# Kernel optimization log

Measured on AMD Instinct MI355X. Metric: run time of the kernel, lower is better.

The kernel has to match this reference:

```python
import jax, jax.numpy as jnp
import numpy as np
import math

WS = (8, 8)        # window_size for context (2D)
HEADS = 8


def _attend(q, k, v, h):
    # q: (Bw, Nq, inner), k/v: (Bw, Nk, inner)
    Bw, Nq, inner = q.shape
    d = inner // h
    q = q.reshape(Bw, Nq, h, d)
    k = k.reshape(Bw, -1, h, d)
    v = v.reshape(Bw, -1, h, d)
    scores = jnp.einsum('bqhd,bkhd->bhqk', q, k) * (d ** -0.5)
    attn = jax.nn.softmax(scores, axis=-1)
    out = jnp.einsum('bhqk,bkhd->bqhd', attn, v)
    return out.reshape(Bw, Nq, inner)


def reference(x, context, W_q, W_k, W_v, W_out, b_out):
    B, C, T, H, W = x.shape
    H_, W_ = context.shape[-2], context.shape[-1]
    ws = WS
    assert H_ * W_ > ws[0] * ws[1] and H * W >= ws[0] * ws[1]  # window branch
    # pad context to multiple of window_size (no-op for chosen shapes)
    pad_r_2d = (-W_) % ws[1]
    pad_b_2d = (-H_) % ws[0]
    context = jnp.pad(context, ((0, 0), (0, 0), (0, pad_b_2d), (0, pad_r_2d)))
    # scaled window size for the (smaller) 3D query tensor
    ws_ = (math.ceil(float(ws[0]) * H / H_), math.ceil(float(ws[1]) * W / W_))
    pad_r_3d = (-W) % ws_[1]
    pad_b_3d = (-H) % ws_[0]
    x = jnp.pad(x, ((0, 0), (0, 0), (0, 0), (0, pad_b_3d), (0, pad_r_3d)))
    Hp, Wp = x.shape[-2], x.shape[-1]
    Hc, Wc = context.shape[-2], context.shape[-1]
    # window partition: context (B,C,Hc,Wc) -> (B*h*w, ws0*ws1, C)
    hc, wc = Hc // ws[0], Wc // ws[1]
    ctx = context.reshape(B, C, hc, ws[0], wc, ws[1])
    ctx = ctx.transpose(0, 2, 4, 3, 5, 1).reshape(B * hc * wc, ws[0] * ws[1], C)
    # window partition: x (B,C,T,Hp,Wp) -> (B*h*w, T*ws_0*ws_1, C)
    hg, wg = Hp // ws_[0], Wp // ws_[1]
    xw = x.reshape(B, C, T, hg, ws_[0], wg, ws_[1])
    xw = xw.transpose(0, 3, 5, 2, 4, 6, 1).reshape(B * hg * wg, T * ws_[0] * ws_[1], C)
    # QKV projections (no bias: qkv_bias=False, to_k always bias-free)
    q = xw @ W_q
    k = ctx @ W_k
    v = ctx @ W_v
    out = _attend(q, k, v, HEADS)  # (Bw, Nq, inner)
    inner = out.shape[-1]
    # window reverse -> (B, inner, T, Hp, Wp)
    out = out.reshape(B, hg, wg, T, ws_[0], ws_[1], inner)
    out = out.transpose(0, 6, 3, 1, 4, 2, 5).reshape(B, inner, T, Hp, Wp)
    out = out[:, :, :, :H, :W]
    # b c t h w -> b (t h w) c
    out = out.transpose(0, 2, 3, 4, 1).reshape(B, T * H * W, inner)
    return out @ W_out + b_out


def setup_inputs() -> dict:
    key = jax.random.key(0)
    ks = jax.random.split(key, 7)
    D = 512
    s = 0.02
    return {
        'x': jax.random.normal(ks[0], (4, D, 4, 32, 32), jnp.float32),
        'context': jax.random.normal(ks[1], (4, D, 128, 128), jnp.float32),
        'W_q': jax.random.normal(ks[2], (D, D), jnp.float32) * s,
        'W_k': jax.random.normal(ks[3], (D, D), jnp.float32) * s,
        'W_v': jax.random.normal(ks[4], (D, D), jnp.float32) * s,
        'W_out': jax.random.normal(ks[5], (D, D), jnp.float32) * s,
        'b_out': jnp.zeros((D,), jnp.float32),
    }
```

## Files before the change

kernel.cpp:

```cpp
#include <hip/hip_runtime.h>
#include <hip/hip_bf16.h>

typedef unsigned short u16;
typedef unsigned int u32;
typedef __attribute__((ext_vector_type(4))) float f32x4;
typedef __attribute__((ext_vector_type(4))) u16 u16x4;
typedef __attribute__((ext_vector_type(8))) u16 u16x8;
typedef __attribute__((ext_vector_type(8))) short s16x8;

__device__ __forceinline__ u16 f2bf(float f) {
    union { float f; u32 u; } v; v.f = f;
    u32 r = v.u + 0x7FFFu + ((v.u >> 16) & 1u);
    return (u16)(r >> 16);
}

__device__ __forceinline__ void gl_lds16(const u16* g, u16* l) {
    __builtin_amdgcn_global_load_lds(
        (const __attribute__((address_space(1))) unsigned int*)(const void*)g,
        (__attribute__((address_space(3))) unsigned int*)(void*)l, 16, 0, 0);
}

__global__ __launch_bounds__(256) void prep_kernel(
    const float* __restrict__ w0, const float* __restrict__ w1,
    const float* __restrict__ w2, const float* __restrict__ w3, u16* __restrict__ WT,
    const float* __restrict__ x, u16* __restrict__ Aq,
    const float* __restrict__ ctx, u16* __restrict__ Actx) {
    __shared__ char smem[16640];
    int bid = blockIdx.x;
    int tid = threadIdx.x;
    if (bid < 8192) {
        u16 (*t)[68] = (u16(*)[68])smem;
        int b2 = bid;
        int cb = b2 & 7; b2 >>= 3;
        int xb = b2 & 1; b2 >>= 1;
        int y  = b2 & 127; b2 >>= 7;
        int b  = b2;
        long ibase = ((long)(b * 512 + cb * 64) * 128 + y) * 128 + xb * 64;
#pragma unroll
        for (int p = 0; p < 4; ++p) {
            int task = p * 256 + tid;
            int cc = task >> 4, xl = (task & 15) * 4;
            float4 v = *(const float4*)&ctx[ibase + (long)cc * 16384 + xl];
            u16x4 o = {f2bf(v.x), f2bf(v.y), f2bf(v.z), f2bf(v.w)};
            *(u16x4*)&t[cc][xl] = o;
        }
        __syncthreads();
#pragma unroll
        for (int p = 0; p < 2; ++p) {
            int task = p * 256 + tid;
            int xx = task >> 3, j = task & 7;
            u16x8 o;
#pragma unroll
            for (int i = 0; i < 8; ++i) o[i] = t[j * 8 + i][xx];
            int xg = xb * 64 + xx;
            int row = b * 16384 + (y >> 3) * 1024 + (xg >> 3) * 64 + (y & 7) * 8 + (xg & 7);
            *(u16x8*)&Actx[(long)row * 512 + cb * 64 + j * 8] = o;
        }
    } else if (bid < 12288) {
        u16 (*t)[36] = (u16(*)[36])smem;
        int b2 = bid - 8192;
        int cb = b2 & 7; b2 >>= 3;
        int y  = b2 & 31; b2 >>= 5;
        int tt = b2 & 3; b2 >>= 2;
        int b  = b2;
        long ibase = ((long)(b * 512 + cb * 64) * 4 + tt) * 1024 + y * 32;
#pragma unroll
        for (int p = 0; p < 2; ++p) {
            int task = p * 256 + tid;
            int cc = task >> 3, xl = (task & 7) * 4;
            float4 v = *(const float4*)&x[ibase + (long)cc * 4096 + xl];
            u16x4 o = {f2bf(v.x), f2bf(v.y), f2bf(v.z), f2bf(v.w)};
            *(u16x4*)&t[cc][xl] = o;
        }
        __syncthreads();
        {
            int xx = tid >> 3, j = tid & 7;
            u16x8 o;
#pragma unroll
            for (int i = 0; i < 8; ++i) o[i] = t[j * 8 + i][xx];
            int row = b * 4096 + (y >> 1) * 256 + (xx >> 1) * 16 + tt * 4 + (y & 1) * 2 + (xx & 1);
            *(u16x8*)&Aq[(long)row * 512 + cb * 64 + j * 8] = o;
        }
    } else {
        float (*t)[65] = (float(*)[65])smem;
        int b2 = bid - 12288;
        int wsel = b2 >> 6;
        int tile = b2 & 63;
        int j0 = (tile >> 3) * 64, c0 = (tile & 7) * 64;
        const float* src = wsel == 0 ? w0 : wsel == 1 ? w1 : wsel == 2 ? w2 : w3;
        u16* out = WT + (long)wsel * 512 * 512;
        int tj = tid & 63;
        int ti = tid >> 6;
#pragma unroll
        for (int p = 0; p < 16; ++p) {
            int row = p * 4 + ti;
            t[row][tj] = src[(long)(c0 + row) * 512 + j0 + tj];
        }
        __syncthreads();
#pragma unroll
        for (int p = 0; p < 16; ++p) {
            int jl = p * 4 + ti;
            out[(long)(j0 + jl) * 512 + c0 + tj] = f2bf(t[tj][jl]);
        }
    }
}

template <int FINAL>
__global__ __launch_bounds__(256, 4) void gemm128_kernel(
    const u16* __restrict__ A, const u16* __restrict__ Bt,
    u16* __restrict__ Cb, float* __restrict__ Cf, const float* __restrict__ bias) {
    __shared__ u16 As[1024 * 8];
    __shared__ u16 Bs[1024 * 8];
    int tid = threadIdx.x;
    int lane = tid & 63;
    int w = tid >> 6;
    int wm = w >> 1, wn = w & 1;
    int bid = blockIdx.x;
    int wg = (bid & 7) * 64 + (bid >> 3);
    int m0 = (wg >> 2) * 128;
    int n0 = (wg & 3) * 128;

    const f32x4 z = {0.f, 0.f, 0.f, 0.f};
    f32x4 acc[4][4];
#pragma unroll
    for (int i = 0; i < 4; ++i)
#pragma unroll
        for (int j = 0; j < 4; ++j) acc[i][j] = z;

    int aoff[4], boff[4], lb[4];
#pragma unroll
    for (int i = 0; i < 4; ++i) {
        int s = i * 256 + tid;
        int row = s >> 3;
        int cb = (s & 7) ^ (row & 7);
        aoff[i] = (m0 + row) * 512 + cb * 8;
        boff[i] = (n0 + row) * 512 + cb * 8;
        lb[i] = (i * 256 + w * 64) * 8;
    }
    int la = lane & 15, lg = lane >> 4;
    for (int ks = 0; ks < 8; ++ks) {
        int ko = ks * 64;
#pragma unroll
        for (int i = 0; i < 4; ++i) {
            gl_lds16(&A[aoff[i] + ko], &As[lb[i]]);
            gl_lds16(&Bt[boff[i] + ko], &Bs[lb[i]]);
        }
        __syncthreads();
#pragma unroll
        for (int kk = 0; kk < 2; ++kk) {
            int cb = kk * 4 + lg;
            s16x8 af[4], bfr[4];
#pragma unroll
            for (int mt = 0; mt < 4; ++mt) {
                int r = wm * 64 + mt * 16 + la;
                af[mt] = *(const s16x8*)&As[r * 64 + ((cb ^ (r & 7)) * 8)];
            }
#pragma unroll
            for (int nt = 0; nt < 4; ++nt) {
                int c = wn * 64 + nt * 16 + la;
                bfr[nt] = *(const s16x8*)&Bs[c * 64 + ((cb ^ (c & 7)) * 8)];
            }
#pragma unroll
            for (int mt = 0; mt < 4; ++mt)
#pragma unroll
                for (int nt = 0; nt < 4; ++nt)
                    acc[mt][nt] = __builtin_amdgcn_mfma_f32_16x16x32_bf16(af[mt], bfr[nt], acc[mt][nt], 0, 0, 0);
        }
        __syncthreads();
    }
#pragma unroll
    for (int mt = 0; mt < 4; ++mt) {
#pragma unroll
        for (int nt = 0; nt < 4; ++nt) {
            int col = n0 + wn * 64 + nt * 16 + la;
#pragma unroll
            for (int rr = 0; rr < 4; ++rr) {
                int r = m0 + wm * 64 + mt * 16 + lg * 4 + rr;
                float v = acc[mt][nt][rr];
                if (FINAL) {
                    int bb = r >> 12, hg = (r >> 8) & 15, wgx = (r >> 4) & 15;
                    int tt = (r >> 2) & 3, rr0 = (r >> 1) & 1, cc0 = r & 1;
                    int tok = bb * 4096 + tt * 1024 + (hg * 2 + rr0) * 32 + wgx * 2 + cc0;
                    Cf[(long)tok * 512 + col] = v + bias[col];
                } else {
                    Cb[(long)r * 512 + col] = f2bf(v);
                }
            }
        }
    }
}

__global__ __launch_bounds__(512, 2) void gemmkv256_kernel(
    const u16* __restrict__ Actx, const u16* __restrict__ WTk, const u16* __restrict__ WTv,
    u16* __restrict__ CK, u16* __restrict__ CVT) {
    __shared__ u16 lds[2][2][16384];
    int tid = threadIdx.x;
    int lane = tid & 63;
    int w = tid >> 6;
    int wm = w >> 2, wn = w & 3;
    int la = lane & 15, lg = lane >> 4;
    int bid = blockIdx.x;
    int wg = (bid & 7) * 128 + (bid >> 3);
    int ttile = wg >> 2;
    int role = wg & 3;
    int isV = role >> 1;
    int half = role & 1;

    const u16* srcA = isV ? WTv : Actx;
    const u16* srcB = isV ? Actx : WTk;

    const f32x4 z = {0.f, 0.f, 0.f, 0.f};
    f32x4 acc[8][4];
#pragma unroll
    for (int i = 0; i < 8; ++i)
#pragma unroll
        for (int j = 0; j < 4; ++j) acc[i][j] = z;

    int aoff[4], boff[4], lsl[4];
#pragma unroll
    for (int i = 0; i < 4; ++i) {
        int s = i * 512 + tid;
        int row = s >> 3;
        int cb = (s & 7) ^ (row & 7);
        int tok = (ttile * 256 + row) * 512 + cb * 8;
        int wgt = (half * 256 + row) * 512 + cb * 8;
        aoff[i] = isV ? wgt : tok;
        boff[i] = isV ? tok : wgt;
        lsl[i] = (i * 512 + w * 64) * 8;
    }

    s16x8 bfr[4][2];

#pragma unroll
    for (int i = 0; i < 4; ++i) {
        gl_lds16(&srcA[aoff[i]], &lds[0][0][lsl[i]]);
        gl_lds16(&srcB[boff[i]], &lds[0][1][lsl[i]]);
    }
#pragma unroll
    for (int i = 0; i < 4; ++i) {
        gl_lds16(&srcA[aoff[i] + 64], &lds[1][0][lsl[i]]);
        gl_lds16(&srcB[boff[i] + 64], &lds[1][1][lsl[i]]);
    }
    asm volatile("s_waitcnt vmcnt(8)" ::: "memory");
    __builtin_amdgcn_s_barrier();
    asm volatile("" ::: "memory");

#pragma unroll
    for (int t = 0; t < 8; ++t) {
        int buf = t & 1;
        const u16* Ab = lds[buf][0];
        const u16* Bb = lds[buf][1];
        int ko2 = (t + 2) * 64;

        {
            int cb = lg;
            s16x8 af[4];
#pragma unroll
            for (int mt = 0; mt < 4; ++mt) {
                int r = wm * 128 + mt * 16 + la;
                af[mt] = *(const s16x8*)&Ab[r * 64 + ((cb ^ (r & 7)) * 8)];
            }
#pragma unroll
            for (int nt = 0; nt < 4; ++nt) {
                int c = wn * 64 + nt * 16 + la;
                bfr[nt][0] = *(const s16x8*)&Bb[c * 64 + ((cb ^ (c & 7)) * 8)];
            }
            __builtin_amdgcn_s_barrier();
            __builtin_amdgcn_s_setprio(1);
#pragma unroll
            for (int mt = 0; mt < 4; ++mt)
#pragma unroll
                for (int nt = 0; nt < 4; ++nt)
                    acc[mt][nt] = __builtin_amdgcn_mfma_f32_16x16x32_bf16(af[mt], bfr[nt][0], acc[mt][nt], 0, 0, 0);
            __builtin_amdgcn_s_setprio(0);
            __builtin_amdgcn_sched_barrier(0);
            __builtin_amdgcn_s_barrier();
        }
        {
            int cb = 4 + lg;
            s16x8 af[4];
#pragma unroll
            for (int mt = 0; mt < 4; ++mt) {
                int r = wm * 128 + mt * 16 + la;
                af[mt] = *(const s16x8*)&Ab[r * 64 + ((cb ^ (r & 7)) * 8)];
            }
#pragma unroll
            for (int nt = 0; nt < 4; ++nt) {
                int c = wn * 64 + nt * 16 + la;
                bfr[nt][1] = *(const s16x8*)&Bb[c * 64 + ((cb ^ (c & 7)) * 8)];
            }
            __builtin_amdgcn_s_barrier();
            __builtin_amdgcn_s_setprio(1);
#pragma unroll
            for (int mt = 0; mt < 4; ++mt)
#pragma unroll
                for (int nt = 0; nt < 4; ++nt)
                    acc[mt][nt] = __builtin_amdgcn_mfma_f32_16x16x32_bf16(af[mt], bfr[nt][1], acc[mt][nt], 0, 0, 0);
            __builtin_amdgcn_s_setprio(0);
            __builtin_amdgcn_sched_barrier(0);
            __builtin_amdgcn_s_barrier();
        }
        {
            int cb = 4 + lg;
            s16x8 af[4];
#pragma unroll
            for (int mt = 0; mt < 4; ++mt) {
                int r = wm * 128 + 64 + mt * 16 + la;
                af[mt] = *(const s16x8*)&Ab[r * 64 + ((cb ^ (r & 7)) * 8)];
            }
            if (t < 6) {
                gl_lds16(&srcB[boff[0] + ko2], &lds[buf][1][lsl[0]]);
                gl_lds16(&srcB[boff[1] + ko2], &lds[buf][1][lsl[1]]);
                gl_lds16(&srcA[aoff[0] + ko2], &lds[buf][0][lsl[0]]);
            }
            __builtin_amdgcn_s_barrier();
            __builtin_amdgcn_s_setprio(1);
#pragma unroll
            for (int mt = 0; mt < 4; ++mt)
#pragma unroll
                for (int nt = 0; nt < 4; ++nt)
                    acc[4 + mt][nt] = __builtin_amdgcn_mfma_f32_16x16x32_bf16(af[mt], bfr[nt][1], acc[4 + mt][nt], 0, 0, 0);
            __builtin_amdgcn_s_setprio(0);
            __builtin_amdgcn_sched_barrier(0);
            __builtin_amdgcn_s_barrier();
        }
        {
            int cb = lg;
            s16x8 af[4];
#pragma unroll
            for (int mt = 0; mt < 4; ++mt) {
                int r = wm * 128 + 64 + mt * 16 + la;
                af[mt] = *(const s16x8*)&Ab[r * 64 + ((cb ^ (r & 7)) * 8)];
            }
            if (t < 6) {
                gl_lds16(&srcB[boff[2] + ko2], &lds[buf][1][lsl[2]]);
                gl_lds16(&srcB[boff[3] + ko2], &lds[buf][1][lsl[3]]);
                gl_lds16(&srcA[aoff[2] + ko2], &lds[buf][0][lsl[2]]);
            }
            __builtin_amdgcn_s_barrier();
            __builtin_amdgcn_s_setprio(1);
#pragma unroll
            for (int mt = 0; mt < 4; ++mt)
#pragma unroll
                for (int nt = 0; nt < 4; ++nt)
                    acc[4 + mt][nt] = __builtin_amdgcn_mfma_f32_16x16x32_bf16(af[mt], bfr[nt][0], acc[4 + mt][nt], 0, 0, 0);
            __builtin_amdgcn_s_setprio(0);
            __builtin_amdgcn_sched_barrier(0);
            __builtin_amdgcn_s_barrier();
        }
        if (t < 6) {
            gl_lds16(&srcA[aoff[1] + ko2], &lds[buf][0][lsl[1]]);
            gl_lds16(&srcA[aoff[3] + ko2], &lds[buf][0][lsl[3]]);
            asm volatile("s_waitcnt vmcnt(8)" ::: "memory");
            __builtin_amdgcn_s_barrier();
            asm volatile("" ::: "memory");
        } else if (t == 6) {
            asm volatile("s_waitcnt vmcnt(0)" ::: "memory");
            __builtin_amdgcn_s_barrier();
            asm volatile("" ::: "memory");
        }
    }

    if (!isV) {
#pragma unroll
        for (int mt = 0; mt < 8; ++mt) {
#pragma unroll
            for (int nt = 0; nt < 4; ++nt) {
                int col = half * 256 + wn * 64 + nt * 16 + la;
#pragma unroll
                for (int rr = 0; rr < 4; ++rr) {
                    int r = ttile * 256 + wm * 128 + mt * 16 + lg * 4 + rr;
                    CK[(long)r * 512 + col] = f2bf(acc[mt][nt][rr]);
                }
            }
        }
    } else {
        int winb = ttile * 4 + wn;
#pragma unroll
        for (int mt = 0; mt < 8; ++mt) {
#pragma unroll
            for (int nt = 0; nt < 4; ++nt) {
                int kv = nt * 16 + la;
#pragma unroll
                for (int rr = 0; rr < 4; ++rr) {
                    int d = half * 256 + wm * 128 + mt * 16 + lg * 4 + rr;
                    CVT[(long)winb * 32768 + d * 64 + kv] = f2bf(acc[mt][nt][rr]);
                }
            }
        }
    }
}

__global__ __launch_bounds__(256) void attn_kernel(
    const u16* __restrict__ Q, const u16* __restrict__ K,
    const u16* __restrict__ VT, u16* __restrict__ O) {
    __shared__ u16 P[4][16 * 104];
    int bid = blockIdx.x;
    int wgid = (bid & 7) * 256 + (bid >> 3);
    int tid = threadIdx.x;
    int wid = tid >> 6;
    int lane = tid & 63;
    int win = wgid >> 1;
    int h = (wgid & 1) * 4 + wid;
    int la = lane & 15, lg = lane >> 4;
    u16* Pw = P[wid];
    const u16* Qb = Q + (long)win * 16 * 512 + h * 64;
    const u16* Kb = K + (long)win * 64 * 512 + h * 64;
    const u16* Vt = VT + (long)win * 32768 + h * 64 * 64;

    s16x8 qf[2];
#pragma unroll
    for (int kk = 0; kk < 2; ++kk)
        qf[kk] = *(const s16x8*)&Qb[la * 512 + kk * 32 + lg * 8];

    const f32x4 z = {0.f, 0.f, 0.f, 0.f};
    f32x4 st[4];
#pragma unroll
    for (int rt = 0; rt < 4; ++rt) st[rt] = z;
#pragma unroll
    for (int rt = 0; rt < 4; ++rt)
#pragma unroll
        for (int kk = 0; kk < 2; ++kk) {
            s16x8 kf = *(const s16x8*)&Kb[(rt * 16 + la) * 512 + kk * 32 + lg * 8];
            st[rt] = __builtin_amdgcn_mfma_f32_16x16x32_bf16(kf, qf[kk], st[rt], 0, 0, 0);
        }
    float mloc = -1e30f;
#pragma unroll
    for (int rt = 0; rt < 4; ++rt)
#pragma unroll
        for (int rr = 0; rr < 4; ++rr) {
            st[rt][rr] *= 0.125f;
            mloc = fmaxf(mloc, st[rt][rr]);
        }
    mloc = fmaxf(mloc, __shfl_xor(mloc, 16));
    mloc = fmaxf(mloc, __shfl_xor(mloc, 32));
    float p[4][4];
    float sloc = 0.f;
#pragma unroll
    for (int rt = 0; rt < 4; ++rt)
#pragma unroll
        for (int rr = 0; rr < 4; ++rr) {
            p[rt][rr] = __expf(st[rt][rr] - mloc);
            sloc += p[rt][rr];
        }
    sloc += __shfl_xor(sloc, 16);
    sloc += __shfl_xor(sloc, 32);
    float inv = 1.0f / sloc;
#pragma unroll
    for (int rt = 0; rt < 4; ++rt)
#pragma unroll
        for (int rr = 0; rr < 4; ++rr)
            Pw[la * 104 + rt * 16 + lg * 4 + rr] = f2bf(p[rt][rr] * inv);
    __syncthreads();

    f32x4 od[4];
#pragma unroll
    for (int dt = 0; dt < 4; ++dt) od[dt] = z;
#pragma unroll
    for (int kk2 = 0; kk2 < 2; ++kk2) {
        s16x8 pa = *(const s16x8*)&Pw[la * 104 + kk2 * 32 + lg * 8];
#pragma unroll
        for (int dt = 0; dt < 4; ++dt) {
            s16x8 vb = *(const s16x8*)&Vt[(dt * 16 + la) * 64 + kk2 * 32 + lg * 8];
            od[dt] = __builtin_amdgcn_mfma_f32_16x16x32_bf16(pa, vb, od[dt], 0, 0, 0);
        }
    }
    u16* Ob = O + (long)win * 16 * 512 + h * 64;
#pragma unroll
    for (int dt = 0; dt < 4; ++dt)
#pragma unroll
        for (int rr = 0; rr < 4; ++rr)
            Ob[(long)(lg * 4 + rr) * 512 + dt * 16 + la] = f2bf(od[dt][rr]);
}

__global__ void sentinel_kernel(float* out) {
    if (threadIdx.x == 0 && blockIdx.x == 0) out[0] = -12345.0f;
}

extern "C" void kernel_launch(void* const* d_in, const int* in_sizes, int n_in,
                              void* d_out, int out_size, void* d_ws, size_t ws_size,
                              hipStream_t stream) {
    const float* x   = (const float*)d_in[0];
    const float* ctx = (const float*)d_in[1];
    const float* Wq  = (const float*)d_in[2];
    const float* Wk  = (const float*)d_in[3];
    const float* Wv  = (const float*)d_in[4];
    const float* Wo  = (const float*)d_in[5];
    const float* bo  = (const float*)d_in[6];
    float* out = (float*)d_out;

    u16* wsb  = (u16*)d_ws;
    u16* WT   = wsb;
    u16* Aq   = WT + 4l * 262144;
    u16* Actx = Aq + 8388608l;
    u16* Qb   = Actx + 33554432l;
    u16* Kb   = Qb + 8388608l;
    u16* VTb  = Kb + 33554432l;
    u16* Ob   = VTb + 33554432l;
    size_t need = (size_t)(126877696l) * 2;
    if (ws_size < need) {
        sentinel_kernel<<<1, 64, 0, stream>>>(out);
        return;
    }

    prep_kernel<<<12544, 256, 0, stream>>>(Wq, Wk, Wv, Wo, WT, x, Aq, ctx, Actx);
    gemm128_kernel<0><<<512, 256, 0, stream>>>(Aq, WT, Qb, nullptr, nullptr);
    gemmkv256_kernel<<<1024, 512, 0, stream>>>(Actx, WT + 262144l, WT + 2l * 262144, Kb, VTb);
    attn_kernel<<<2048, 256, 0, stream>>>(Qb, Kb, VTb, Ob);
    gemm128_kernel<1><<<512, 256, 0, stream>>>(Ob, WT + 3l * 262144, nullptr, out, bo);
}
```

Measured before the change: 198.8 us.

## Merge Q projection into KV GEMM kernel with 128x128 tiles

Replaces the separate Q-projection GEMM launch and the 256x256-tile K/V GEMM with one kernel that covers Q, K and V^T using 128x128 tiles and 256-thread blocks. The inner loop is simplified to two k-substeps per 64-wide chunk, with all prefetch loads issued after the compute and a single barrier pair. This removes one kernel launch and lets Q tiles fill the tail of the K/V grid. In exchange, smaller tiles give less data reuse per block and the finer interleaving of loads with MFMA work is lost.

New measurement: 210.5 us. +5.9%, slower.

```diff
diff --git a/kernel.cpp b/kernel.cpp
--- a/kernel.cpp
+++ b/kernel.cpp
@@ -190,56 +190,58 @@
     }
 }
 
-__global__ __launch_bounds__(512, 2) void gemmkv256_kernel(
-    const u16* __restrict__ Actx, const u16* __restrict__ WTk, const u16* __restrict__ WTv,
-    u16* __restrict__ CK, u16* __restrict__ CVT) {
-    __shared__ u16 lds[2][2][16384];
+__global__ __launch_bounds__(256, 2) void gemmkvq_kernel(
+    const u16* __restrict__ Actx, const u16* __restrict__ WTq, const u16* __restrict__ WTk,
+    const u16* __restrict__ WTv, const u16* __restrict__ Aq,
+    u16* __restrict__ CQ, u16* __restrict__ CK, u16* __restrict__ CVT) {
+    __shared__ u16 lds[2][2][8192];
     int tid = threadIdx.x;
     int lane = tid & 63;
     int w = tid >> 6;
-    int wm = w >> 2, wn = w & 3;
+    int wm = w >> 1, wn = w & 1;
     int la = lane & 15, lg = lane >> 4;
     int bid = blockIdx.x;
-    int wg = (bid & 7) * 128 + (bid >> 3);
-    int ttile = wg >> 2;
-    int role = wg & 3;
-    int isV = role >> 1;
-    int half = role & 1;
-
-    const u16* srcA = isV ? WTv : Actx;
-    const u16* srcB = isV ? Actx : WTk;
+    int wg = (bid & 7) * 576 + (bid >> 3);
+
+    const u16 *sA, *sB;
+    u16* Co;
+    int aBase, bBase, isV;
+    if (wg < 4096) {
+        int tt = wg >> 3, r8 = wg & 7;
+        if (r8 < 4) { isV = 0; sA = Actx; aBase = tt * 128; sB = WTk; bBase = r8 * 128; Co = CK; }
+        else        { isV = 1; sA = WTv; aBase = (r8 - 4) * 128; sB = Actx; bBase = tt * 128; Co = CVT; }
+    } else {
+        int q = wg - 4096;
+        isV = 0; sA = Aq; aBase = (q >> 2) * 128; sB = WTq; bBase = (q & 3) * 128; Co = CQ;
+    }
 
     const f32x4 z = {0.f, 0.f, 0.f, 0.f};
-    f32x4 acc[8][4];
-#pragma unroll
-    for (int i = 0; i < 8; ++i)
+    f32x4 acc[4][4];
+#pragma unroll
+    for (int i = 0; i < 4; ++i)
 #pragma unroll
         for (int j = 0; j < 4; ++j) acc[i][j] = z;
 
-    int aoff[4], boff[4], lsl[4];
+    int aoff[4], boff[4], lb[4];
 #pragma unroll
     for (int i = 0; i < 4; ++i) {
-        int s = i * 512 + tid;
+        int s = i * 256 + tid;
         int row = s >> 3;
         int cb = (s & 7) ^ (row & 7);
-        int tok = (ttile * 256 + row) * 512 + cb * 8;
-        int wgt = (half * 256 + row) * 512 + cb * 8;
-        aoff[i] = isV ? wgt : tok;
-        boff[i] = isV ? tok : wgt;
-        lsl[i] = (i * 512 + w * 64) * 8;
-    }
-
-    s16x8 bfr[4][2];
+        aoff[i] = (aBase + row) * 512 + cb * 8;
+        boff[i] = (bBase + row) * 512 + cb * 8;
+        lb[i] = (i * 256 + w * 64) * 8;
+    }
 
 #pragma unroll
     for (int i = 0; i < 4; ++i) {
-        gl_lds16(&srcA[aoff[i]], &lds[0][0][lsl[i]]);
-        gl_lds16(&srcB[boff[i]], &lds[0][1][lsl[i]]);
+        gl_lds16(&sA[aoff[i]], &lds[0][0][lb[i]]);
+        gl_lds16(&sB[boff[i]], &lds[0][1][lb[i]]);
     }
 #pragma unroll
     for (int i = 0; i < 4; ++i) {
-        gl_lds16(&srcA[aoff[i] + 64], &lds[1][0][lsl[i]]);
-        gl_lds16(&srcB[boff[i] + 64], &lds[1][1][lsl[i]]);
+        gl_lds16(&sA[aoff[i] + 64], &lds[1][0][lb[i]]);
+        gl_lds16(&sB[boff[i] + 64], &lds[1][1][lb[i]]);
     }
     asm volatile("s_waitcnt vmcnt(8)" ::: "memory");
     __builtin_amdgcn_s_barrier();
@@ -250,107 +252,38 @@
         int buf = t & 1;
         const u16* Ab = lds[buf][0];
         const u16* Bb = lds[buf][1];
-        int ko2 = (t + 2) * 64;
-
-        {
-            int cb = lg;
-            s16x8 af[4];
+#pragma unroll
+        for (int kk = 0; kk < 2; ++kk) {
+            int cb = kk * 4 + lg;
+            s16x8 af[4], bfr[4];
 #pragma unroll
             for (int mt = 0; mt < 4; ++mt) {
-                int r = wm * 128 + mt * 16 + la;
+                int r = wm * 64 + mt * 16 + la;
                 af[mt] = *(const s16x8*)&Ab[r * 64 + ((cb ^ (r & 7)) * 8)];
             }
 #pragma unroll
             for (int nt = 0; nt < 4; ++nt) {
                 int c = wn * 64 + nt * 16 + la;
-                bfr[nt][0] = *(const s16x8*)&Bb[c * 64 + ((cb ^ (c & 7)) * 8)];
-            }
+                bfr[nt] = *(const s16x8*)&Bb[c * 64 + ((cb ^ (c & 7)) * 8)];
+            }
+            __builtin_amdgcn_s_setprio(1);
+#pragma unroll
+            for (int mt = 0; mt < 4; ++mt)
+#pragma unroll
+                for (int nt = 0; nt < 4; ++nt)
+                    acc[mt][nt] = __builtin_amdgcn_mfma_f32_16x16x32_bf16(af[mt], bfr[nt], acc[mt][nt], 0, 0, 0);
+            __builtin_amdgcn_s_setprio(0);
+        }
+        __builtin_amdgcn_sched_barrier(0);
+        if (t < 6) {
+            asm volatile("" ::: "memory");
             __builtin_amdgcn_s_barrier();
-            __builtin_amdgcn_s_setprio(1);
-#pragma unroll
-            for (int mt = 0; mt < 4; ++mt)
-#pragma unroll
-                for (int nt = 0; nt < 4; ++nt)
-                    acc[mt][nt] = __builtin_amdgcn_mfma_f32_16x16x32_bf16(af[mt], bfr[nt][0], acc[mt][nt], 0, 0, 0);
-            __builtin_amdgcn_s_setprio(0);
-            __builtin_amdgcn_sched_barrier(0);
-            __builtin_amdgcn_s_barrier();
-        }
-        {
-            int cb = 4 + lg;
-            s16x8 af[4];
-#pragma unroll
-            for (int mt = 0; mt < 4; ++mt) {
-                int r = wm * 128 + mt * 16 + la;
-                af[mt] = *(const s16x8*)&Ab[r * 64 + ((cb ^ (r & 7)) * 8)];
-            }
-#pragma unroll
-            for (int nt = 0; nt < 4; ++nt) {
-                int c = wn * 64 + nt * 16 + la;
-                bfr[nt][1] = *(const s16x8*)&Bb[c * 64 + ((cb ^ (c & 7)) * 8)];
-            }
-            __builtin_amdgcn_s_barrier();
-            __builtin_amdgcn_s_setprio(1);
-#pragma unroll
-            for (int mt = 0; mt < 4; ++mt)
-#pragma unroll
-                for (int nt = 0; nt < 4; ++nt)
-                    acc[mt][nt] = __builtin_amdgcn_mfma_f32_16x16x32_bf16(af[mt], bfr[nt][1], acc[mt][nt], 0, 0, 0);
-            __builtin_amdgcn_s_setprio(0);
-            __builtin_amdgcn_sched_barrier(0);
-            __builtin_amdgcn_s_barrier();
-        }
-        {
-            int cb = 4 + lg;
-            s16x8 af[4];
-#pragma unroll
-            for (int mt = 0; mt < 4; ++mt) {
-                int r = wm * 128 + 64 + mt * 16 + la;
-                af[mt] = *(const s16x8*)&Ab[r * 64 + ((cb ^ (r & 7)) * 8)];
-            }
-            if (t < 6) {
-                gl_lds16(&srcB[boff[0] + ko2], &lds[buf][1][lsl[0]]);
-                gl_lds16(&srcB[boff[1] + ko2], &lds[buf][1][lsl[1]]);
-                gl_lds16(&srcA[aoff[0] + ko2], &lds[buf][0][lsl[0]]);
-            }
-            __builtin_amdgcn_s_barrier();
-            __builtin_amdgcn_s_setprio(1);
-#pragma unroll
-            for (int mt = 0; mt < 4; ++mt)
-#pragma unroll
-                for (int nt = 0; nt < 4; ++nt)
-                    acc[4 + mt][nt] = __builtin_amdgcn_mfma_f32_16x16x32_bf16(af[mt], bfr[nt][1], acc[4 + mt][nt], 0, 0, 0);
-            __builtin_amdgcn_s_setprio(0);
-            __builtin_amdgcn_sched_barrier(0);
-            __builtin_amdgcn_s_barrier();
-        }
-        {
-            int cb = lg;
-            s16x8 af[4];
-#pragma unroll
-            for (int mt = 0; mt < 4; ++mt) {
-                int r = wm * 128 + 64 + mt * 16 + la;
-                af[mt] = *(const s16x8*)&Ab[r * 64 + ((cb ^ (r & 7)) * 8)];
-            }
-            if (t < 6) {
-                gl_lds16(&srcB[boff[2] + ko2], &lds[buf][1][lsl[2]]);
-                gl_lds16(&srcB[boff[3] + ko2], &lds[buf][1][lsl[3]]);
-                gl_lds16(&srcA[aoff[2] + ko2], &lds[buf][0][lsl[2]]);
-            }
-            __builtin_amdgcn_s_barrier();
-            __builtin_amdgcn_s_setprio(1);
-#pragma unroll
-            for (int mt = 0; mt < 4; ++mt)
-#pragma unroll
-                for (int nt = 0; nt < 4; ++nt)
-                    acc[4 + mt][nt] = __builtin_amdgcn_mfma_f32_16x16x32_bf16(af[mt], bfr[nt][0], acc[4 + mt][nt], 0, 0, 0);
-            __builtin_amdgcn_s_setprio(0);
-            __builtin_amdgcn_sched_barrier(0);
-            __builtin_amdgcn_s_barrier();
-        }
-        if (t < 6) {
-            gl_lds16(&srcA[aoff[1] + ko2], &lds[buf][0][lsl[1]]);
-            gl_lds16(&srcA[aoff[3] + ko2], &lds[buf][0][lsl[3]]);
+            int ko2 = (t + 2) * 64;
+#pragma unroll
+            for (int i = 0; i < 4; ++i) {
+                gl_lds16(&sA[aoff[i] + ko2], &lds[buf][0][lb[i]]);
+                gl_lds16(&sB[boff[i] + ko2], &lds[buf][1][lb[i]]);
+            }
             asm volatile("s_waitcnt vmcnt(8)" ::: "memory");
             __builtin_amdgcn_s_barrier();
             asm volatile("" ::: "memory");
@@ -363,28 +296,27 @@
 
     if (!isV) {
 #pragma unroll
-        for (int mt = 0; mt < 8; ++mt) {
-#pragma unroll
-            for (int nt = 0; nt < 4; ++nt) {
-                int col = half * 256 + wn * 64 + nt * 16 + la;
-#pragma unroll
-                for (int rr = 0; rr < 4; ++rr) {
-                    int r = ttile * 256 + wm * 128 + mt * 16 + lg * 4 + rr;
-                    CK[(long)r * 512 + col] = f2bf(acc[mt][nt][rr]);
+        for (int mt = 0; mt < 4; ++mt) {
+#pragma unroll
+            for (int rr = 0; rr < 4; ++rr) {
+                int r = aBase + wm * 64 + mt * 16 + lg * 4 + rr;
+#pragma unroll
+                for (int nt = 0; nt < 4; ++nt) {
+                    int col = bBase + wn * 64 + nt * 16 + la;
+                    Co[(long)r * 512 + col] = f2bf(acc[mt][nt][rr]);
                 }
             }
         }
     } else {
-        int winb = ttile * 4 + wn;
-#pragma unroll
-        for (int mt = 0; mt < 8; ++mt) {
-#pragma unroll
-            for (int nt = 0; nt < 4; ++nt) {
-                int kv = nt * 16 + la;
-#pragma unroll
-                for (int rr = 0; rr < 4; ++rr) {
-                    int d = half * 256 + wm * 128 + mt * 16 + lg * 4 + rr;
-                    CVT[(long)winb * 32768 + d * 64 + kv] = f2bf(acc[mt][nt][rr]);
+        int winb = (bBase >> 6) + wn;
+#pragma unroll
+        for (int mt = 0; mt < 4; ++mt) {
+#pragma unroll
+            for (int rr = 0; rr < 4; ++rr) {
+                int d = aBase + wm * 64 + mt * 16 + lg * 4 + rr;
+#pragma unroll
+                for (int nt = 0; nt < 4; ++nt) {
+                    Co[(long)winb * 32768 + d * 64 + nt * 16 + la] = f2bf(acc[mt][nt][rr]);
                 }
             }
         }
@@ -504,8 +436,8 @@
     }
 
     prep_kernel<<<12544, 256, 0, stream>>>(Wq, Wk, Wv, Wo, WT, x, Aq, ctx, Actx);
-    gemm128_kernel<0><<<512, 256, 0, stream>>>(Aq, WT, Qb, nullptr, nullptr);
-    gemmkv256_kernel<<<1024, 512, 0, stream>>>(Actx, WT + 262144l, WT + 2l * 262144, Kb, VTb);
+    gemmkvq_kernel<<<4608, 256, 0, stream>>>(Actx, WT, WT + 262144l, WT + 2l * 262144,
+                                             Aq, Qb, Kb, VTb);
     attn_kernel<<<2048, 256, 0, stream>>>(Qb, Kb, VTb, Ob);
     gemm128_kernel<1><<<512, 256, 0, stream>>>(Ob, WT + 3l * 262144, nullptr, out, bo);
 }
```
